# Kernel tuning notes

Hardware: AMD Instinct MI355X
Metric: run time of the kernel (lower is better)

## Reference

```python
import jax, jax.numpy as jnp
import numpy as np

B, S, D_MODEL, D_ATTN, H, F = 4, 2048, 512, 512, 8, 4
DEPTH = D_ATTN // H


def setup_inputs() -> dict:
    key = jax.random.key(0)
    ks = jax.random.split(key, 14)
    s = 0.02
    return {
        "q": jax.random.normal(ks[0], (B, S, D_MODEL), jnp.float32),
        "k": jax.random.normal(ks[1], (B, S, D_MODEL), jnp.float32),
        "v": jax.random.normal(ks[2], (B, S, D_MODEL), jnp.float32),
        "xdiff": jax.random.normal(ks[3], (B, S, S, F), jnp.float32),
        "wq": jax.random.normal(ks[4], (D_MODEL, D_ATTN), jnp.float32) * s,
        "bq": jnp.zeros((D_ATTN,), jnp.float32),
        "wk": jax.random.normal(ks[5], (D_MODEL, D_ATTN), jnp.float32) * s,
        "bk": jnp.zeros((D_ATTN,), jnp.float32),
        "wv": jax.random.normal(ks[6], (D_MODEL, D_ATTN), jnp.float32) * s,
        "bv": jnp.zeros((D_ATTN,), jnp.float32),
        "wx": jax.random.normal(ks[7], (D_ATTN, H * F), jnp.float32) * s,
        "bx": jnp.zeros((H * F,), jnp.float32),
        "wo": jax.random.normal(ks[8], (D_ATTN, D_MODEL), jnp.float32) * s,
        "bo": jnp.zeros((D_MODEL,), jnp.float32),
    }


def reference(q, k, v, xdiff, wq, bq, wk, bk, wv, bv, wx, bx, wo, bo):
    # projections
    qp = q @ wq + bq            # [B, Sq, D_ATTN]
    kp = k @ wk + bk            # [B, Sk, D_ATTN]
    vp = v @ wv + bv            # [B, Sk, D_ATTN]
    x = qp @ wx + bx            # [B, Sq, H*F]
    x = x.reshape(B, S, H, F)   # [B, Sq, H, F]

    # split heads -> [B, H, S, depth]
    def split_heads(t):
        return t.reshape(B, S, H, DEPTH).transpose(0, 2, 1, 3)

    qh, kh, vh = split_heads(qp), split_heads(kp), split_heads(vp)

    # xdiff bias: [B, Sq, Sk, F] x [B, Sq, H, F] -> [B, H, Sq, Sk]
    bias = jnp.einsum('bqkf,bqhf->bhqk', xdiff, x) / jnp.sqrt(jnp.float32(F))

    logits = jnp.einsum('bhqd,bhkd->bhqk', qh, kh) / jnp.sqrt(jnp.float32(DEPTH)) + bias
    attn = jax.nn.softmax(logits, axis=-1)              # [B, H, Sq, Sk]
    out = jnp.einsum('bhqk,bhkd->bhqd', attn, vh)       # [B, H, Sq, depth]
    out = out.transpose(0, 2, 1, 3).reshape(B, S, D_ATTN)
    out = out @ wo + bo                                  # [B, Sq, D_MODEL]
    return out, attn
```

## Files before the change

kernel.cpp:

```cpp
#include <hip/hip_runtime.h>
#include <stdint.h>

#define S_LEN 2048
#define NB 4
#define NH 8
#define KC_A 4
#define KC_B 2

typedef __attribute__((ext_vector_type(8))) short s8v;
typedef __attribute__((ext_vector_type(4))) float f4v;

#define MFMA16(a, b, c) __builtin_amdgcn_mfma_f32_16x16x32_bf16((a), (b), (c), 0, 0, 0)

static __device__ __forceinline__ unsigned short f2bf(float f) {
    unsigned int u = __builtin_bit_cast(unsigned int, f);
    u += 0x7fffu + ((u >> 16) & 1u);
    return (unsigned short)(u >> 16);
}
static __device__ __forceinline__ float bf2f(unsigned short h) {
    unsigned int u = ((unsigned int)h) << 16;
    return __builtin_bit_cast(float, u);
}

__global__ __launch_bounds__(256) void wprep(const float* __restrict__ W,
                                             unsigned short* __restrict__ Wt)
{
    __shared__ float tile[16][17];
    const int tx = threadIdx.x, ty = threadIdx.y;
    const int n0 = blockIdx.x * 16, k0 = blockIdx.y * 16;
    tile[ty][tx] = W[(size_t)(k0 + ty) * 512 + n0 + tx];
    __syncthreads();
    Wt[(size_t)(n0 + ty) * 512 + k0 + tx] = f2bf(tile[tx][ty]);
}

template <int MODE, int ASRC>
__global__ __launch_bounds__(256) void gemm_tile(
    const void* __restrict__ Av, const unsigned short* __restrict__ Wt,
    const float* __restrict__ bias, void* __restrict__ Cv)
{
    __shared__ unsigned short a_lds[64 * 32];
    __shared__ unsigned short wt_lds[64 * 32];
    const int t = threadIdx.x;
    const int w = t >> 6, lane = t & 63;
    const int quad = lane >> 4, l15 = lane & 15;
    const int m0 = blockIdx.x * 64, n0 = blockIdx.y * 64;

    f4v acc[4] = {};
    const int srow = t >> 2, sc8 = (t & 3) * 8;

    for (int k0 = 0; k0 < 512; k0 += 32) {
        __syncthreads();
        if constexpr (ASRC == 0) {
            const float* ap = (const float*)Av + (size_t)(m0 + srow) * 512 + k0 + sc8;
            f4v v0 = *(const f4v*)ap;
            f4v v1 = *(const f4v*)(ap + 4);
            *(ushort4*)&a_lds[srow * 32 + sc8] =
                make_ushort4(f2bf(v0[0]), f2bf(v0[1]), f2bf(v0[2]), f2bf(v0[3]));
            *(ushort4*)&a_lds[srow * 32 + sc8 + 4] =
                make_ushort4(f2bf(v1[0]), f2bf(v1[1]), f2bf(v1[2]), f2bf(v1[3]));
        } else {
            const float* a0 = (const float*)Av + (size_t)(m0 + srow) * 512 + k0 + sc8;
            const float* a1 = a0 + (size_t)8192 * 512;
            f4v v0 = *(const f4v*)a0 + *(const f4v*)a1;
            f4v v1 = *(const f4v*)(a0 + 4) + *(const f4v*)(a1 + 4);
            *(ushort4*)&a_lds[srow * 32 + sc8] =
                make_ushort4(f2bf(v0[0]), f2bf(v0[1]), f2bf(v0[2]), f2bf(v0[3]));
            *(ushort4*)&a_lds[srow * 32 + sc8 + 4] =
                make_ushort4(f2bf(v1[0]), f2bf(v1[1]), f2bf(v1[2]), f2bf(v1[3]));
        }
        *(uint4*)&wt_lds[srow * 32 + sc8] =
            *(const uint4*)(Wt + (size_t)(n0 + srow) * 512 + k0 + sc8);
        __syncthreads();
        s8v wf = *(const s8v*)&wt_lds[(w * 16 + l15) * 32 + quad * 8];
        #pragma unroll
        for (int rt = 0; rt < 4; ++rt) {
            s8v af = *(const s8v*)&a_lds[(rt * 16 + l15) * 32 + quad * 8];
            acc[rt] = MFMA16(af, wf, acc[rt]);
        }
    }

    const float bv = bias[n0 + w * 16 + l15];
    const int n = n0 + w * 16 + l15;
    #pragma unroll
    for (int rt = 0; rt < 4; ++rt) {
        const int mb = m0 + rt * 16 + quad * 4;
        if constexpr (MODE == 0) {
            unsigned short* C = (unsigned short*)Cv;
            #pragma unroll
            for (int r = 0; r < 4; ++r)
                C[(size_t)(mb + r) * 512 + n] = f2bf(acc[rt][r] + bv);
        } else if constexpr (MODE == 1) {
            unsigned short* C = (unsigned short*)Cv;
            ushort4 u = make_ushort4(f2bf(acc[rt][0] + bv), f2bf(acc[rt][1] + bv),
                                     f2bf(acc[rt][2] + bv), f2bf(acc[rt][3] + bv));
            *(ushort4*)&C[(size_t)(mb >> 11) * (512 * 2048) + (size_t)n * 2048 + (mb & 2047)] = u;
        } else {
            float* C = (float*)Cv;
            #pragma unroll
            for (int r = 0; r < 4; ++r)
                C[(size_t)(mb + r) * 512 + n] = acc[rt][r] + bv;
        }
    }
}

__global__ __launch_bounds__(256) void xproj_kernel(
    const unsigned short* __restrict__ qp, const float* __restrict__ wx,
    const float* __restrict__ bx, float* __restrict__ xout)
{
    __shared__ unsigned short qrow[8 * 512];
    const int t = threadIdx.x;
    const size_t base = (size_t)blockIdx.x * 8 * 512;
    #pragma unroll
    for (int i = 0; i < 2; ++i) {
        const int idx = (i * 256 + t) * 8;
        *(uint4*)&qrow[idx] = *(const uint4*)&qp[base + idx];
    }
    __syncthreads();
    const int r = t >> 5, j = t & 31;
    float acc = bx[j];
    #pragma unroll 8
    for (int d = 0; d < 512; ++d)
        acc = fmaf(bf2f(qrow[r * 512 + d]), wx[d * 32 + j], acc);
    xout[(size_t)blockIdx.x * 256 + t] = acc;
}

__global__ __launch_bounds__(256) void attn_sums(
    const unsigned short* __restrict__ qp, const unsigned short* __restrict__ kp,
    const float* __restrict__ xws, const float* __restrict__ xdiff,
    float* __restrict__ lpart)
{
    __shared__ float x_lds[16 * 32];
    const int t = threadIdx.x, w = t >> 6, lane = t & 63;
    const int quad = lane >> 4, l15 = lane & 15;
    const int b = blockIdx.y, q0 = blockIdx.x * 16, kc = blockIdx.z;
    const int h0 = 2 * w;

    {
        const float* src = xws + ((size_t)(b * S_LEN) + q0) * 32;
        x_lds[t] = src[t];
        x_lds[t + 256] = src[t + 256];
    }
    __syncthreads();

    s8v qf[2][2];
    #pragma unroll
    for (int e = 0; e < 2; ++e)
        #pragma unroll
        for (int kk = 0; kk < 2; ++kk)
            qf[e][kk] = *(const s8v*)&qp[((size_t)(b * S_LEN + q0 + l15)) * 512 +
                                         (h0 + e) * 64 + kk * 32 + quad * 8];
    f4v xh[2][4];
    #pragma unroll
    for (int e = 0; e < 2; ++e)
        #pragma unroll
        for (int r = 0; r < 4; ++r)
            xh[e][r] = *(const f4v*)&x_lds[(quad * 4 + r) * 32 + (h0 + e) * 4];

    const size_t kp_base = (size_t)b * S_LEN * 512;
    const size_t xd_base = ((size_t)(b * S_LEN) + q0) * S_LEN * 4;

    float lp[2][4] = {};
    const int kbeg = kc * (S_LEN / KC_A);
    for (int k0 = kbeg; k0 < kbeg + S_LEN / KC_A; k0 += 32) {
        s8v kf[2][2][2];
        #pragma unroll
        for (int e = 0; e < 2; ++e)
            #pragma unroll
            for (int kt = 0; kt < 2; ++kt)
                #pragma unroll
                for (int kk = 0; kk < 2; ++kk)
                    kf[e][kt][kk] = *(const s8v*)&kp[kp_base +
                        (size_t)(k0 + kt * 16 + l15) * 512 + (h0 + e) * 64 + kk * 32 + quad * 8];
        f4v xd[2][4];
        #pragma unroll
        for (int kt = 0; kt < 2; ++kt)
            #pragma unroll
            for (int r = 0; r < 4; ++r)
                xd[kt][r] = *(const f4v*)&xdiff[xd_base +
                    ((size_t)(quad * 4 + r) * S_LEN + k0 + kt * 16 + l15) * 4];

        #pragma unroll
        for (int e = 0; e < 2; ++e) {
            #pragma unroll
            for (int kt = 0; kt < 2; ++kt) {
                f4v c = {0.f, 0.f, 0.f, 0.f};
                c = MFMA16(qf[e][0], kf[e][kt][0], c);
                c = MFMA16(qf[e][1], kf[e][kt][1], c);
                #pragma unroll
                for (int r = 0; r < 4; ++r) {
                    float bias4 = xd[kt][r][0] * xh[e][r][0] + xd[kt][r][1] * xh[e][r][1] +
                                  xd[kt][r][2] * xh[e][r][2] + xd[kt][r][3] * xh[e][r][3];
                    float lg = c[r] * 0.125f + bias4 * 0.5f;
                    lp[e][r] += __expf(lg);
                }
            }
        }
    }

    #pragma unroll
    for (int e = 0; e < 2; ++e)
        #pragma unroll
        for (int r = 0; r < 4; ++r) {
            float s = lp[e][r];
            s += __shfl_xor(s, 1);
            s += __shfl_xor(s, 2);
            s += __shfl_xor(s, 4);
            s += __shfl_xor(s, 8);
            if (l15 == 0)
                lpart[(((size_t)kc * NB + b) * NH + h0 + e) * S_LEN + q0 + quad * 4 + r] = s;
        }
}

__global__ __launch_bounds__(256) void attn_pv(
    const unsigned short* __restrict__ qp, const unsigned short* __restrict__ kp,
    const unsigned short* __restrict__ vT, const float* __restrict__ xws,
    const float* __restrict__ xdiff, const float* __restrict__ lpart,
    float* __restrict__ attn, float* __restrict__ opart)
{
    __shared__ float x_lds[16 * 32];
    __shared__ unsigned short p_lds[4 * 2 * 16 * 32];
    const int t = threadIdx.x, w = t >> 6, lane = t & 63;
    const int quad = lane >> 4, l15 = lane & 15;
    const int b = blockIdx.y, q0 = blockIdx.x * 16, kcb = blockIdx.z;
    const int h0 = 2 * w;

    {
        const float* src = xws + ((size_t)(b * S_LEN) + q0) * 32;
        x_lds[t] = src[t];
        x_lds[t + 256] = src[t + 256];
    }
    __syncthreads();

    s8v qf[2][2];
    #pragma unroll
    for (int e = 0; e < 2; ++e)
        #pragma unroll
        for (int kk = 0; kk < 2; ++kk)
            qf[e][kk] = *(const s8v*)&qp[((size_t)(b * S_LEN + q0 + l15)) * 512 +
                                         (h0 + e) * 64 + kk * 32 + quad * 8];
    f4v xh[2][4];
    #pragma unroll
    for (int e = 0; e < 2; ++e)
        #pragma unroll
        for (int r = 0; r < 4; ++r)
            xh[e][r] = *(const f4v*)&x_lds[(quad * 4 + r) * 32 + (h0 + e) * 4];

    const size_t kp_base = (size_t)b * S_LEN * 512;
    const size_t xd_base = ((size_t)(b * S_LEN) + q0) * S_LEN * 4;
    const size_t vt_base = (size_t)b * 512 * S_LEN;

    float rinv[2][4];
    #pragma unroll
    for (int e = 0; e < 2; ++e)
        #pragma unroll
        for (int r = 0; r < 4; ++r) {
            const int row = q0 + quad * 4 + r;
            float s = 0.f;
            #pragma unroll
            for (int kc = 0; kc < KC_A; ++kc)
                s += lpart[(((size_t)kc * NB + b) * NH + h0 + e) * S_LEN + row];
            rinv[e][r] = 1.0f / s;
        }

    f4v oacc[2][4] = {};
    const int kbeg = kcb * (S_LEN / KC_B);
    for (int k0 = kbeg; k0 < kbeg + S_LEN / KC_B; k0 += 32) {
        s8v kf[2][2][2];
        #pragma unroll
        for (int e = 0; e < 2; ++e)
            #pragma unroll
            for (int kt = 0; kt < 2; ++kt)
                #pragma unroll
                for (int kk = 0; kk < 2; ++kk)
                    kf[e][kt][kk] = *(const s8v*)&kp[kp_base +
                        (size_t)(k0 + kt * 16 + l15) * 512 + (h0 + e) * 64 + kk * 32 + quad * 8];
        f4v xd[2][4];
        #pragma unroll
        for (int kt = 0; kt < 2; ++kt)
            #pragma unroll
            for (int r = 0; r < 4; ++r)
                xd[kt][r] = *(const f4v*)&xdiff[xd_base +
                    ((size_t)(quad * 4 + r) * S_LEN + k0 + kt * 16 + l15) * 4];

        #pragma unroll
        for (int e = 0; e < 2; ++e) {
            #pragma unroll
            for (int kt = 0; kt < 2; ++kt) {
                f4v c = {0.f, 0.f, 0.f, 0.f};
                c = MFMA16(qf[e][0], kf[e][kt][0], c);
                c = MFMA16(qf[e][1], kf[e][kt][1], c);
                #pragma unroll
                for (int r = 0; r < 4; ++r) {
                    float bias4 = xd[kt][r][0] * xh[e][r][0] + xd[kt][r][1] * xh[e][r][1] +
                                  xd[kt][r][2] * xh[e][r][2] + xd[kt][r][3] * xh[e][r][3];
                    float lg = c[r] * 0.125f + bias4 * 0.5f;
                    float P = __expf(lg) * rinv[e][r];
                    size_t aidx = ((size_t)((b * NH + h0 + e) * S_LEN) + q0 + quad * 4 + r) * S_LEN +
                                  k0 + kt * 16 + l15;
                    __builtin_nontemporal_store(P, &attn[aidx]);
                    p_lds[((w * 2 + e) * 16 + quad * 4 + r) * 32 + kt * 16 + l15] = f2bf(P);
                }
            }
            s8v pa = *(const s8v*)&p_lds[((w * 2 + e) * 16 + l15) * 32 + quad * 8];
            #pragma unroll
            for (int dt = 0; dt < 4; ++dt) {
                s8v vf = *(const s8v*)&vT[vt_base +
                    (size_t)((h0 + e) * 64 + dt * 16 + l15) * S_LEN + k0 + quad * 8];
                oacc[e][dt] = MFMA16(pa, vf, oacc[e][dt]);
            }
        }
    }

    #pragma unroll
    for (int e = 0; e < 2; ++e)
        #pragma unroll
        for (int dt = 0; dt < 4; ++dt)
            #pragma unroll
            for (int r = 0; r < 4; ++r)
                opart[((size_t)kcb * 8192 + b * S_LEN + q0 + quad * 4 + r) * 512 +
                      (h0 + e) * 64 + dt * 16 + l15] = oacc[e][dt][r];
}

extern "C" void kernel_launch(void* const* d_in, const int* in_sizes, int n_in,
                              void* d_out, int out_size, void* d_ws, size_t ws_size,
                              hipStream_t stream) {
    const float* q     = (const float*)d_in[0];
    const float* k     = (const float*)d_in[1];
    const float* v     = (const float*)d_in[2];
    const float* xdiff = (const float*)d_in[3];
    const float* wq    = (const float*)d_in[4];
    const float* bq    = (const float*)d_in[5];
    const float* wk    = (const float*)d_in[6];
    const float* bk    = (const float*)d_in[7];
    const float* wv    = (const float*)d_in[8];
    const float* bv    = (const float*)d_in[9];
    const float* wx    = (const float*)d_in[10];
    const float* bx    = (const float*)d_in[11];
    const float* wo    = (const float*)d_in[12];
    const float* bo    = (const float*)d_in[13];

    float* outp = (float*)d_out;
    float* attn = outp + (size_t)NB * S_LEN * 512;

    const size_t MK = (size_t)8192 * 512;
    const size_t WSZ = (size_t)512 * 512;
    unsigned short* qp   = (unsigned short*)d_ws;
    unsigned short* kpw  = qp + MK;
    unsigned short* vT   = kpw + MK;
    unsigned short* wtq  = vT + MK;
    unsigned short* wtk  = wtq + WSZ;
    unsigned short* wtv  = wtk + WSZ;
    unsigned short* wto  = wtv + WSZ;
    float* xws   = (float*)(wto + WSZ);
    float* lpart = xws + (size_t)8192 * 32;
    float* opart = lpart + (size_t)KC_A * NB * NH * S_LEN;

    dim3 wg(32, 32), wb(16, 16);
    wprep<<<wg, wb, 0, stream>>>(wq, wtq);
    wprep<<<wg, wb, 0, stream>>>(wk, wtk);
    wprep<<<wg, wb, 0, stream>>>(wv, wtv);
    wprep<<<wg, wb, 0, stream>>>(wo, wto);

    dim3 gg(128, 8);
    gemm_tile<0, 0><<<gg, 256, 0, stream>>>(q, wtq, bq, qp);
    gemm_tile<0, 0><<<gg, 256, 0, stream>>>(k, wtk, bk, kpw);
    gemm_tile<1, 0><<<gg, 256, 0, stream>>>(v, wtv, bv, vT);
    xproj_kernel<<<1024, 256, 0, stream>>>(qp, wx, bx, xws);

    attn_sums<<<dim3(128, NB, KC_A), 256, 0, stream>>>(qp, kpw, xws, xdiff, lpart);
    attn_pv<<<dim3(128, NB, KC_B), 256, 0, stream>>>(qp, kpw, vT, xws, xdiff, lpart, attn, opart);

    gemm_tile<2, 2><<<gg, 256, 0, stream>>>(opart, wto, bo, outp);
}
```

Before: 1.360 ms.

## Stage xdiff tiles via async global-to-LDS loads, one head per wave, fuse launches

The attention kernels now use 512 threads with one head per wave. The xdiff bias tile for 16 queries by 64 keys is staged into double-buffered LDS with global_load_lds, so all 8 heads share one load instead of each wave re-reading it from global memory. The weight-prep and Q/K/V projection launches are merged into single grid-z-indexed kernels to cut launch overhead. This adds a block-wide barrier per 64-key tile and raises LDS use per block, which may limit occupancy.

```diff
diff --git a/kernel.cpp b/kernel.cpp
--- a/kernel.cpp
+++ b/kernel.cpp
@@ -22,10 +22,27 @@
     return __builtin_bit_cast(float, u);
 }
 
-__global__ __launch_bounds__(256) void wprep(const float* __restrict__ W,
-                                             unsigned short* __restrict__ Wt)
+static __device__ __forceinline__ void gload_lds16(const void* gsrc, void* ldst) {
+    __builtin_amdgcn_global_load_lds(
+        (const __attribute__((address_space(1))) unsigned int*)gsrc,
+        (__attribute__((address_space(3))) unsigned int*)ldst, 16, 0, 0);
+}
+
+__global__ __launch_bounds__(256) void wprep4(
+    const float* __restrict__ w0, const float* __restrict__ w1,
+    const float* __restrict__ w2, const float* __restrict__ w3,
+    unsigned short* __restrict__ t0, unsigned short* __restrict__ t1,
+    unsigned short* __restrict__ t2, unsigned short* __restrict__ t3)
 {
     __shared__ float tile[16][17];
+    const float* W;
+    unsigned short* Wt;
+    switch (blockIdx.z) {
+        case 0: W = w0; Wt = t0; break;
+        case 1: W = w1; Wt = t1; break;
+        case 2: W = w2; Wt = t2; break;
+        default: W = w3; Wt = t3; break;
+    }
     const int tx = threadIdx.x, ty = threadIdx.y;
     const int n0 = blockIdx.x * 16, k0 = blockIdx.y * 16;
     tile[ty][tx] = W[(size_t)(k0 + ty) * 512 + n0 + tx];
@@ -34,7 +51,7 @@
 }
 
 template <int MODE, int ASRC>
-__global__ __launch_bounds__(256) void gemm_tile(
+static __device__ __forceinline__ void gemm_body(
     const void* __restrict__ Av, const unsigned short* __restrict__ Wt,
     const float* __restrict__ bias, void* __restrict__ Cv)
 {
@@ -103,6 +120,26 @@
     }
 }
 
+__global__ __launch_bounds__(256) void gemm3(
+    const float* __restrict__ q, const float* __restrict__ k, const float* __restrict__ v,
+    const unsigned short* __restrict__ wtq, const unsigned short* __restrict__ wtk,
+    const unsigned short* __restrict__ wtv,
+    const float* __restrict__ bq, const float* __restrict__ bk, const float* __restrict__ bv,
+    unsigned short* __restrict__ qp, unsigned short* __restrict__ kpw,
+    unsigned short* __restrict__ vT)
+{
+    if (blockIdx.z == 0) gemm_body<0, 0>(q, wtq, bq, qp);
+    else if (blockIdx.z == 1) gemm_body<0, 0>(k, wtk, bk, kpw);
+    else gemm_body<1, 0>(v, wtv, bv, vT);
+}
+
+__global__ __launch_bounds__(256) void gemm_final(
+    const float* __restrict__ opart, const unsigned short* __restrict__ wto,
+    const float* __restrict__ bo, float* __restrict__ outp)
+{
+    gemm_body<2, 2>(opart, wto, bo, outp);
+}
+
 __global__ __launch_bounds__(256) void xproj_kernel(
     const unsigned short* __restrict__ qp, const float* __restrict__ wx,
     const float* __restrict__ bx, float* __restrict__ xout)
@@ -124,201 +161,191 @@
     xout[(size_t)blockIdx.x * 256 + t] = acc;
 }
 
-__global__ __launch_bounds__(256) void attn_sums(
+__global__ __launch_bounds__(512, 4) void attn_sums(
     const unsigned short* __restrict__ qp, const unsigned short* __restrict__ kp,
     const float* __restrict__ xws, const float* __restrict__ xdiff,
     float* __restrict__ lpart)
 {
-    __shared__ float x_lds[16 * 32];
+    __shared__ float xtile[2][16 * 64 * 4];
     const int t = threadIdx.x, w = t >> 6, lane = t & 63;
     const int quad = lane >> 4, l15 = lane & 15;
     const int b = blockIdx.y, q0 = blockIdx.x * 16, kc = blockIdx.z;
-    const int h0 = 2 * w;
-
-    {
-        const float* src = xws + ((size_t)(b * S_LEN) + q0) * 32;
-        x_lds[t] = src[t];
-        x_lds[t + 256] = src[t + 256];
-    }
-    __syncthreads();
-
-    s8v qf[2][2];
-    #pragma unroll
-    for (int e = 0; e < 2; ++e)
-        #pragma unroll
-        for (int kk = 0; kk < 2; ++kk)
-            qf[e][kk] = *(const s8v*)&qp[((size_t)(b * S_LEN + q0 + l15)) * 512 +
-                                         (h0 + e) * 64 + kk * 32 + quad * 8];
-    f4v xh[2][4];
-    #pragma unroll
-    for (int e = 0; e < 2; ++e)
-        #pragma unroll
-        for (int r = 0; r < 4; ++r)
-            xh[e][r] = *(const f4v*)&x_lds[(quad * 4 + r) * 32 + (h0 + e) * 4];
+    const int h = w;
+
+    s8v qf[2];
+    #pragma unroll
+    for (int kk = 0; kk < 2; ++kk)
+        qf[kk] = *(const s8v*)&qp[((size_t)(b * S_LEN + q0 + l15)) * 512 +
+                                  h * 64 + kk * 32 + quad * 8];
+    f4v xh[4];
+    #pragma unroll
+    for (int r = 0; r < 4; ++r)
+        xh[r] = *(const f4v*)&xws[((size_t)(b * S_LEN + q0 + quad * 4 + r)) * 32 + h * 4];
 
     const size_t kp_base = (size_t)b * S_LEN * 512;
-    const size_t xd_base = ((size_t)(b * S_LEN) + q0) * S_LEN * 4;
-
-    float lp[2][4] = {};
+    const size_t xd_base = ((size_t)(b * S_LEN + q0)) * S_LEN * 4;
+
+    float lp[4] = {};
     const int kbeg = kc * (S_LEN / KC_A);
-    for (int k0 = kbeg; k0 < kbeg + S_LEN / KC_A; k0 += 32) {
-        s8v kf[2][2][2];
-        #pragma unroll
-        for (int e = 0; e < 2; ++e)
+    const int nt = (S_LEN / KC_A) / 64;
+
+    #pragma unroll
+    for (int j = 0; j < 2; ++j)
+        gload_lds16(xdiff + xd_base + (size_t)(w * 2 + j) * (S_LEN * 4) + (size_t)(kbeg + lane) * 4,
+                    &xtile[0][(w * 2 + j) * 256]);
+
+    for (int tix = 0; tix < nt; ++tix) {
+        __syncthreads();
+        const int k0 = kbeg + tix * 64;
+        if (tix + 1 < nt) {
+            #pragma unroll
+            for (int j = 0; j < 2; ++j)
+                gload_lds16(xdiff + xd_base + (size_t)(w * 2 + j) * (S_LEN * 4) +
+                                (size_t)(k0 + 64 + lane) * 4,
+                            &xtile[(tix + 1) & 1][(w * 2 + j) * 256]);
+        }
+        const float* xt = xtile[tix & 1];
+
+        #pragma unroll
+        for (int ks = 0; ks < 2; ++ks) {
+            const int kk0 = k0 + ks * 32;
+            s8v kf[2][2];
             #pragma unroll
             for (int kt = 0; kt < 2; ++kt)
                 #pragma unroll
                 for (int kk = 0; kk < 2; ++kk)
-                    kf[e][kt][kk] = *(const s8v*)&kp[kp_base +
-                        (size_t)(k0 + kt * 16 + l15) * 512 + (h0 + e) * 64 + kk * 32 + quad * 8];
-        f4v xd[2][4];
-        #pragma unroll
-        for (int kt = 0; kt < 2; ++kt)
-            #pragma unroll
-            for (int r = 0; r < 4; ++r)
-                xd[kt][r] = *(const f4v*)&xdiff[xd_base +
-                    ((size_t)(quad * 4 + r) * S_LEN + k0 + kt * 16 + l15) * 4];
-
-        #pragma unroll
-        for (int e = 0; e < 2; ++e) {
+                    kf[kt][kk] = *(const s8v*)&kp[kp_base +
+                        (size_t)(kk0 + kt * 16 + l15) * 512 + h * 64 + kk * 32 + quad * 8];
             #pragma unroll
             for (int kt = 0; kt < 2; ++kt) {
                 f4v c = {0.f, 0.f, 0.f, 0.f};
-                c = MFMA16(qf[e][0], kf[e][kt][0], c);
-                c = MFMA16(qf[e][1], kf[e][kt][1], c);
+                c = MFMA16(qf[0], kf[kt][0], c);
+                c = MFMA16(qf[1], kf[kt][1], c);
                 #pragma unroll
                 for (int r = 0; r < 4; ++r) {
-                    float bias4 = xd[kt][r][0] * xh[e][r][0] + xd[kt][r][1] * xh[e][r][1] +
-                                  xd[kt][r][2] * xh[e][r][2] + xd[kt][r][3] * xh[e][r][3];
-                    float lg = c[r] * 0.125f + bias4 * 0.5f;
-                    lp[e][r] += __expf(lg);
+                    f4v xd = *(const f4v*)&xt[((quad * 4 + r) * 64 + ks * 32 + kt * 16 + l15) * 4];
+                    float bias4 = xd[0] * xh[r][0] + xd[1] * xh[r][1] +
+                                  xd[2] * xh[r][2] + xd[3] * xh[r][3];
+                    lp[r] += __expf(c[r] * 0.125f + bias4 * 0.5f);
                 }
             }
         }
     }
 
     #pragma unroll
-    for (int e = 0; e < 2; ++e)
-        #pragma unroll
-        for (int r = 0; r < 4; ++r) {
-            float s = lp[e][r];
-            s += __shfl_xor(s, 1);
-            s += __shfl_xor(s, 2);
-            s += __shfl_xor(s, 4);
-            s += __shfl_xor(s, 8);
-            if (l15 == 0)
-                lpart[(((size_t)kc * NB + b) * NH + h0 + e) * S_LEN + q0 + quad * 4 + r] = s;
-        }
-}
-
-__global__ __launch_bounds__(256) void attn_pv(
+    for (int r = 0; r < 4; ++r) {
+        float s = lp[r];
+        s += __shfl_xor(s, 1);
+        s += __shfl_xor(s, 2);
+        s += __shfl_xor(s, 4);
+        s += __shfl_xor(s, 8);
+        if (l15 == 0)
+            lpart[(((size_t)kc * NB + b) * NH + h) * S_LEN + q0 + quad * 4 + r] = s;
+    }
+}
+
+__global__ __launch_bounds__(512, 4) void attn_pv(
     const unsigned short* __restrict__ qp, const unsigned short* __restrict__ kp,
     const unsigned short* __restrict__ vT, const float* __restrict__ xws,
     const float* __restrict__ xdiff, const float* __restrict__ lpart,
     float* __restrict__ attn, float* __restrict__ opart)
 {
-    __shared__ float x_lds[16 * 32];
-    __shared__ unsigned short p_lds[4 * 2 * 16 * 32];
+    __shared__ float xtile[2][16 * 64 * 4];
+    __shared__ unsigned short p_lds[8 * 16 * 32];
     const int t = threadIdx.x, w = t >> 6, lane = t & 63;
     const int quad = lane >> 4, l15 = lane & 15;
     const int b = blockIdx.y, q0 = blockIdx.x * 16, kcb = blockIdx.z;
-    const int h0 = 2 * w;
-
-    {
-        const float* src = xws + ((size_t)(b * S_LEN) + q0) * 32;
-        x_lds[t] = src[t];
-        x_lds[t + 256] = src[t + 256];
-    }
-    __syncthreads();
-
-    s8v qf[2][2];
-    #pragma unroll
-    for (int e = 0; e < 2; ++e)
-        #pragma unroll
-        for (int kk = 0; kk < 2; ++kk)
-            qf[e][kk] = *(const s8v*)&qp[((size_t)(b * S_LEN + q0 + l15)) * 512 +
-                                         (h0 + e) * 64 + kk * 32 + quad * 8];
-    f4v xh[2][4];
-    #pragma unroll
-    for (int e = 0; e < 2; ++e)
-        #pragma unroll
-        for (int r = 0; r < 4; ++r)
-            xh[e][r] = *(const f4v*)&x_lds[(quad * 4 + r) * 32 + (h0 + e) * 4];
+    const int h = w;
+
+    s8v qf[2];
+    #pragma unroll
+    for (int kk = 0; kk < 2; ++kk)
+        qf[kk] = *(const s8v*)&qp[((size_t)(b * S_LEN + q0 + l15)) * 512 +
+                                  h * 64 + kk * 32 + quad * 8];
+    f4v xh[4];
+    #pragma unroll
+    for (int r = 0; r < 4; ++r)
+        xh[r] = *(const f4v*)&xws[((size_t)(b * S_LEN + q0 + quad * 4 + r)) * 32 + h * 4];
+
+    float rinv[4];
+    #pragma unroll
+    for (int r = 0; r < 4; ++r) {
+        const int row = q0 + quad * 4 + r;
+        float s = 0.f;
+        #pragma unroll
+        for (int kc = 0; kc < KC_A; ++kc)
+            s += lpart[(((size_t)kc * NB + b) * NH + h) * S_LEN + row];
+        rinv[r] = 1.0f / s;
+    }
 
     const size_t kp_base = (size_t)b * S_LEN * 512;
-    const size_t xd_base = ((size_t)(b * S_LEN) + q0) * S_LEN * 4;
+    const size_t xd_base = ((size_t)(b * S_LEN + q0)) * S_LEN * 4;
     const size_t vt_base = (size_t)b * 512 * S_LEN;
-
-    float rinv[2][4];
-    #pragma unroll
-    for (int e = 0; e < 2; ++e)
-        #pragma unroll
-        for (int r = 0; r < 4; ++r) {
-            const int row = q0 + quad * 4 + r;
-            float s = 0.f;
-            #pragma unroll
-            for (int kc = 0; kc < KC_A; ++kc)
-                s += lpart[(((size_t)kc * NB + b) * NH + h0 + e) * S_LEN + row];
-            rinv[e][r] = 1.0f / s;
-        }
-
-    f4v oacc[2][4] = {};
+    const size_t attn_row = ((size_t)((b * NH + h) * S_LEN) + q0) * S_LEN;
+
+    f4v oacc[4] = {};
     const int kbeg = kcb * (S_LEN / KC_B);
-    for (int k0 = kbeg; k0 < kbeg + S_LEN / KC_B; k0 += 32) {
-        s8v kf[2][2][2];
-        #pragma unroll
-        for (int e = 0; e < 2; ++e)
+    const int nt = (S_LEN / KC_B) / 64;
+
+    #pragma unroll
+    for (int j = 0; j < 2; ++j)
+        gload_lds16(xdiff + xd_base + (size_t)(w * 2 + j) * (S_LEN * 4) + (size_t)(kbeg + lane) * 4,
+                    &xtile[0][(w * 2 + j) * 256]);
+
+    for (int tix = 0; tix < nt; ++tix) {
+        __syncthreads();
+        const int k0 = kbeg + tix * 64;
+        if (tix + 1 < nt) {
+            #pragma unroll
+            for (int j = 0; j < 2; ++j)
+                gload_lds16(xdiff + xd_base + (size_t)(w * 2 + j) * (S_LEN * 4) +
+                                (size_t)(k0 + 64 + lane) * 4,
+                            &xtile[(tix + 1) & 1][(w * 2 + j) * 256]);
+        }
+        const float* xt = xtile[tix & 1];
+
+        #pragma unroll
+        for (int ks = 0; ks < 2; ++ks) {
+            const int kk0 = k0 + ks * 32;
+            s8v kf[2][2];
             #pragma unroll
             for (int kt = 0; kt < 2; ++kt)
                 #pragma unroll
                 for (int kk = 0; kk < 2; ++kk)
-                    kf[e][kt][kk] = *(const s8v*)&kp[kp_base +
-                        (size_t)(k0 + kt * 16 + l15) * 512 + (h0 + e) * 64 + kk * 32 + quad * 8];
-        f4v xd[2][4];
-        #pragma unroll
-        for (int kt = 0; kt < 2; ++kt)
-            #pragma unroll
-            for (int r = 0; r < 4; ++r)
-                xd[kt][r] = *(const f4v*)&xdiff[xd_base +
-                    ((size_t)(quad * 4 + r) * S_LEN + k0 + kt * 16 + l15) * 4];
-
-        #pragma unroll
-        for (int e = 0; e < 2; ++e) {
+                    kf[kt][kk] = *(const s8v*)&kp[kp_base +
+                        (size_t)(kk0 + kt * 16 + l15) * 512 + h * 64 + kk * 32 + quad * 8];
             #pragma unroll
             for (int kt = 0; kt < 2; ++kt) {
                 f4v c = {0.f, 0.f, 0.f, 0.f};
-                c = MFMA16(qf[e][0], kf[e][kt][0], c);
-                c = MFMA16(qf[e][1], kf[e][kt][1], c);
+                c = MFMA16(qf[0], kf[kt][0], c);
+                c = MFMA16(qf[1], kf[kt][1], c);
                 #pragma unroll
                 for (int r = 0; r < 4; ++r) {
-                    float bias4 = xd[kt][r][0] * xh[e][r][0] + xd[kt][r][1] * xh[e][r][1] +
-                                  xd[kt][r][2] * xh[e][r][2] + xd[kt][r][3] * xh[e][r][3];
-                    float lg = c[r] * 0.125f + bias4 * 0.5f;
-                    float P = __expf(lg) * rinv[e][r];
-                    size_t aidx = ((size_t)((b * NH + h0 + e) * S_LEN) + q0 + quad * 4 + r) * S_LEN +
-                                  k0 + kt * 16 + l15;
-                    __builtin_nontemporal_store(P, &attn[aidx]);
-                    p_lds[((w * 2 + e) * 16 + quad * 4 + r) * 32 + kt * 16 + l15] = f2bf(P);
+                    f4v xd = *(const f4v*)&xt[((quad * 4 + r) * 64 + ks * 32 + kt * 16 + l15) * 4];
+                    float bias4 = xd[0] * xh[r][0] + xd[1] * xh[r][1] +
+                                  xd[2] * xh[r][2] + xd[3] * xh[r][3];
+                    float P = __expf(c[r] * 0.125f + bias4 * 0.5f) * rinv[r];
+                    __builtin_nontemporal_store(P,
+                        &attn[attn_row + (size_t)(quad * 4 + r) * S_LEN + kk0 + kt * 16 + l15]);
+                    p_lds[(h * 16 + quad * 4 + r) * 32 + kt * 16 + l15] = f2bf(P);
                 }
             }
-            s8v pa = *(const s8v*)&p_lds[((w * 2 + e) * 16 + l15) * 32 + quad * 8];
+            s8v pa = *(const s8v*)&p_lds[(h * 16 + l15) * 32 + quad * 8];
             #pragma unroll
             for (int dt = 0; dt < 4; ++dt) {
                 s8v vf = *(const s8v*)&vT[vt_base +
-                    (size_t)((h0 + e) * 64 + dt * 16 + l15) * S_LEN + k0 + quad * 8];
-                oacc[e][dt] = MFMA16(pa, vf, oacc[e][dt]);
+                    (size_t)(h * 64 + dt * 16 + l15) * S_LEN + kk0 + quad * 8];
+                oacc[dt] = MFMA16(pa, vf, oacc[dt]);
             }
         }
     }
 
     #pragma unroll
-    for (int e = 0; e < 2; ++e)
-        #pragma unroll
-        for (int dt = 0; dt < 4; ++dt)
-            #pragma unroll
-            for (int r = 0; r < 4; ++r)
-                opart[((size_t)kcb * 8192 + b * S_LEN + q0 + quad * 4 + r) * 512 +
-                      (h0 + e) * 64 + dt * 16 + l15] = oacc[e][dt][r];
+    for (int dt = 0; dt < 4; ++dt)
+        #pragma unroll
+        for (int r = 0; r < 4; ++r)
+            opart[((size_t)kcb * 8192 + b * S_LEN + q0 + quad * 4 + r) * 512 +
+                  h * 64 + dt * 16 + l15] = oacc[dt][r];
 }
 
 extern "C" void kernel_launch(void* const* d_in, const int* in_sizes, int n_in,
@@ -355,20 +382,12 @@
     float* lpart = xws + (size_t)8192 * 32;
     float* opart = lpart + (size_t)KC_A * NB * NH * S_LEN;
 
-    dim3 wg(32, 32), wb(16, 16);
-    wprep<<<wg, wb, 0, stream>>>(wq, wtq);
-    wprep<<<wg, wb, 0, stream>>>(wk, wtk);
-    wprep<<<wg, wb, 0, stream>>>(wv, wtv);
-    wprep<<<wg, wb, 0, stream>>>(wo, wto);
-
-    dim3 gg(128, 8);
-    gemm_tile<0, 0><<<gg, 256, 0, stream>>>(q, wtq, bq, qp);
-    gemm_tile<0, 0><<<gg, 256, 0, stream>>>(k, wtk, bk, kpw);
-    gemm_tile<1, 0><<<gg, 256, 0, stream>>>(v, wtv, bv, vT);
+    wprep4<<<dim3(32, 32, 4), dim3(16, 16), 0, stream>>>(wq, wk, wv, wo, wtq, wtk, wtv, wto);
+    gemm3<<<dim3(128, 8, 3), 256, 0, stream>>>(q, k, v, wtq, wtk, wtv, bq, bk, bv, qp, kpw, vT);
     xproj_kernel<<<1024, 256, 0, stream>>>(qp, wx, bx, xws);
 
-    attn_sums<<<dim3(128, NB, KC_A), 256, 0, stream>>>(qp, kpw, xws, xdiff, lpart);
-    attn_pv<<<dim3(128, NB, KC_B), 256, 0, stream>>>(qp, kpw, vT, xws, xdiff, lpart, attn, opart);
-
-    gemm_tile<2, 2><<<gg, 256, 0, stream>>>(opart, wto, bo, outp);
-}
+    attn_sums<<<dim3(128, NB, KC_A), 512, 0, stream>>>(qp, kpw, xws, xdiff, lpart);
+    attn_pv<<<dim3(128, NB, KC_B), 512, 0, stream>>>(qp, kpw, vT, xws, xdiff, lpart, attn, opart);
+
+    gemm_final<<<dim3(128, 8), 256, 0, stream>>>(opart, wto, bo, outp);
+}
```

Result: faster. 1.313 ms (-3.5%).
